# Kernel tuning notes

Measured on AMD Instinct MI355X. Metric: run time of the kernel, lower is better.

## Reference

```python
import jax, jax.numpy as jnp
import numpy as np

EPS = 1e-10


def setup_inputs() -> dict:
    key = jax.random.key(0)
    k1, k2, k3 = jax.random.split(key, 3)
    B, V = 256, 128000
    logits = jax.random.normal(k1, (B, V), dtype=jnp.float32)
    # temperatures in (0,1]; set a few entries to exactly 0 to exercise the greedy branch
    temps = jax.random.uniform(k2, (B,), dtype=jnp.float32)
    temps = temps.at[::16].set(0.0)
    # exponential(1) noise, matching torch.empty_like(probs).exponential_(1)
    exp_noise = jax.random.exponential(k3, (B, V), dtype=jnp.float32)
    return {"logits": logits, "temperatures": temps, "exp_noise": exp_noise}


def reference(logits, temperatures, exp_noise):
    logits = logits.astype(jnp.float32)
    greedy_tokens = jnp.argmax(logits, axis=-1)  # [B]
    # avoid 0-division; rows with temp==0 are overridden by the greedy branch anyway
    safe_t = jnp.where(temperatures == 0.0, 1.0, temperatures)[:, None]  # [B,1]
    probs = jax.nn.softmax(logits / safe_t, axis=-1)  # [B,V]
    # Gumbel-max style sampling: argmax of probs / Exp(1) noise
    sample_tokens = jnp.argmax(probs / (exp_noise + EPS), axis=-1)  # [B]
    return jnp.where(temperatures == 0.0, greedy_tokens, sample_tokens)
```

## Files before the change

kernel.cpp:

```cpp
#include <hip/hip_runtime.h>
#include <math.h>


__device__ __forceinline__ void amax_combine(float& v, int& i, float ov, int oi) {
    if (ov > v || (ov == v && oi < i)) { v = ov; i = oi; }
}

__global__ __launch_bounds__(1024) void draft_sampler_kernel(
    const float* __restrict__ logits,
    const float* __restrict__ temps,
    const float* __restrict__ noise,
    int* __restrict__ out,
    int V)
{
    const int row = blockIdx.x;
    const int tid = threadIdx.x;
    const int nthr = blockDim.x;
    const int lane = tid & 63;
    const int wid  = tid >> 6;
    const int nwaves = nthr >> 6;

    const size_t base = (size_t)row * (size_t)V;
    const float4* l4 = (const float4*)(logits + base);
    const int n4 = V >> 2;

    __shared__ float sv[16];
    __shared__ int   si[16];

    float bv = -INFINITY; int bi = 0x7fffffff;
    for (int j = tid; j < n4; j += nthr) {
        float4 x = l4[j];
        int k = j << 2;
        if (x.x > bv) { bv = x.x; bi = k; }
        if (x.y > bv) { bv = x.y; bi = k + 1; }
        if (x.z > bv) { bv = x.z; bi = k + 2; }
        if (x.w > bv) { bv = x.w; bi = k + 3; }
    }
    #pragma unroll
    for (int off = 32; off > 0; off >>= 1) {
        float ov = __shfl_down(bv, off, 64);
        int   oi = __shfl_down(bi, off, 64);
        amax_combine(bv, bi, ov, oi);
    }
    if (lane == 0) { sv[wid] = bv; si[wid] = bi; }
    __syncthreads();
    if (tid == 0) {
        float gv = sv[0]; int gi = si[0];
        for (int w = 1; w < nwaves; ++w) amax_combine(gv, gi, sv[w], si[w]);
        sv[0] = gv; si[0] = gi;
    }
    __syncthreads();
    const float gmax = sv[0];
    const int   gidx = si[0];

    const float t = temps[row];
    if (t == 0.0f) {
        if (tid == 0) out[row] = gidx;
        return;
    }
    const float xm = gmax / t;
    const float4* z4 = (const float4*)(noise + base);

    float rv = -INFINITY; int ri = 0x7fffffff;
    for (int j = tid; j < n4; j += nthr) {
        float4 x = l4[j];
        float4 z = z4[j];
        int k = j << 2;
        float r0 = expf(x.x / t - xm) / (z.x + 1e-10f);
        float r1 = expf(x.y / t - xm) / (z.y + 1e-10f);
        float r2 = expf(x.z / t - xm) / (z.z + 1e-10f);
        float r3 = expf(x.w / t - xm) / (z.w + 1e-10f);
        if (r0 > rv) { rv = r0; ri = k; }
        if (r1 > rv) { rv = r1; ri = k + 1; }
        if (r2 > rv) { rv = r2; ri = k + 2; }
        if (r3 > rv) { rv = r3; ri = k + 3; }
    }
    #pragma unroll
    for (int off = 32; off > 0; off >>= 1) {
        float ov = __shfl_down(rv, off, 64);
        int   oi = __shfl_down(ri, off, 64);
        amax_combine(rv, ri, ov, oi);
    }
    __syncthreads();
    if (lane == 0) { sv[wid] = rv; si[wid] = ri; }
    __syncthreads();
    if (tid == 0) {
        float gv = sv[0]; int gi = si[0];
        for (int w = 1; w < nwaves; ++w) amax_combine(gv, gi, sv[w], si[w]);
        out[row] = gi;
    }
}

extern "C" void kernel_launch(void* const* d_in, const int* in_sizes, int n_in,
                              void* d_out, int out_size, void* d_ws, size_t ws_size,
                              hipStream_t stream) {
    const float* logits = (const float*)d_in[0];
    const float* temps  = (const float*)d_in[1];
    const float* noise  = (const float*)d_in[2];
    int* out = (int*)d_out;

    const int B = in_sizes[1];
    const int V = in_sizes[0] / B;

    draft_sampler_kernel<<<B, 1024, 0, stream>>>(logits, temps, noise, out, V);
}
```

Measured before the change: 279.2 us.

## Rewrite Gumbel sampling in log space with fused single pass and split-row reduction

Replaces exp-softmax-divide with an equivalent log-domain score x*(1/t)*log2e - log2(z), so the row max is no longer needed. Greedy and sampled argmax are computed in the same single pass over logits and noise, which drops the second read of the logits. Each row is split across 8 blocks of 256 threads, with per-segment partial results written to a workspace and combined by a small second kernel. It uses fast __log2f, which may change argmax results on near-ties.

```diff
diff --git a/kernel.cpp b/kernel.cpp
--- a/kernel.cpp
+++ b/kernel.cpp
@@ -1,94 +1,106 @@
 #include <hip/hip_runtime.h>
 #include <math.h>
 
+
+#define SEGS 8
 
 __device__ __forceinline__ void amax_combine(float& v, int& i, float ov, int oi) {
     if (ov > v || (ov == v && oi < i)) { v = ov; i = oi; }
 }
 
-__global__ __launch_bounds__(1024) void draft_sampler_kernel(
+__global__ __launch_bounds__(256) void draft_pass1(
     const float* __restrict__ logits,
     const float* __restrict__ temps,
     const float* __restrict__ noise,
-    int* __restrict__ out,
+    float4* __restrict__ ws,
     int V)
 {
-    const int row = blockIdx.x;
+    const int seg = blockIdx.x;
+    const int row = blockIdx.y;
     const int tid = threadIdx.x;
-    const int nthr = blockDim.x;
     const int lane = tid & 63;
     const int wid  = tid >> 6;
-    const int nwaves = nthr >> 6;
+
+    const int n4  = V >> 2;
+    const int per = n4 / SEGS;
+    const int j0  = seg * per;
+    const int j1  = (seg == SEGS - 1) ? n4 : (j0 + per);
+
+    const float t = temps[row];
+    const float safe_t = (t == 0.0f) ? 1.0f : t;
+    const float c = (1.0f / safe_t) * 1.4426950408889634f;
 
     const size_t base = (size_t)row * (size_t)V;
     const float4* l4 = (const float4*)(logits + base);
-    const int n4 = V >> 2;
-
-    __shared__ float sv[16];
-    __shared__ int   si[16];
-
-    float bv = -INFINITY; int bi = 0x7fffffff;
-    for (int j = tid; j < n4; j += nthr) {
-        float4 x = l4[j];
-        int k = j << 2;
-        if (x.x > bv) { bv = x.x; bi = k; }
-        if (x.y > bv) { bv = x.y; bi = k + 1; }
-        if (x.z > bv) { bv = x.z; bi = k + 2; }
-        if (x.w > bv) { bv = x.w; bi = k + 3; }
-    }
-    #pragma unroll
-    for (int off = 32; off > 0; off >>= 1) {
-        float ov = __shfl_down(bv, off, 64);
-        int   oi = __shfl_down(bi, off, 64);
-        amax_combine(bv, bi, ov, oi);
-    }
-    if (lane == 0) { sv[wid] = bv; si[wid] = bi; }
-    __syncthreads();
-    if (tid == 0) {
-        float gv = sv[0]; int gi = si[0];
-        for (int w = 1; w < nwaves; ++w) amax_combine(gv, gi, sv[w], si[w]);
-        sv[0] = gv; si[0] = gi;
-    }
-    __syncthreads();
-    const float gmax = sv[0];
-    const int   gidx = si[0];
-
-    const float t = temps[row];
-    if (t == 0.0f) {
-        if (tid == 0) out[row] = gidx;
-        return;
-    }
-    const float xm = gmax / t;
     const float4* z4 = (const float4*)(noise + base);
 
-    float rv = -INFINITY; int ri = 0x7fffffff;
-    for (int j = tid; j < n4; j += nthr) {
+    float gv = -INFINITY; int gi = 0x7fffffff;
+    float sv = -INFINITY; int si = 0x7fffffff;
+
+    for (int j = j0 + tid; j < j1; j += 256) {
         float4 x = l4[j];
         float4 z = z4[j];
         int k = j << 2;
-        float r0 = expf(x.x / t - xm) / (z.x + 1e-10f);
-        float r1 = expf(x.y / t - xm) / (z.y + 1e-10f);
-        float r2 = expf(x.z / t - xm) / (z.z + 1e-10f);
-        float r3 = expf(x.w / t - xm) / (z.w + 1e-10f);
-        if (r0 > rv) { rv = r0; ri = k; }
-        if (r1 > rv) { rv = r1; ri = k + 1; }
-        if (r2 > rv) { rv = r2; ri = k + 2; }
-        if (r3 > rv) { rv = r3; ri = k + 3; }
+        if (x.x > gv) { gv = x.x; gi = k;     }
+        if (x.y > gv) { gv = x.y; gi = k + 1; }
+        if (x.z > gv) { gv = x.z; gi = k + 2; }
+        if (x.w > gv) { gv = x.w; gi = k + 3; }
+        float s0 = fmaf(x.x, c, -__log2f(z.x + 1e-10f));
+        float s1 = fmaf(x.y, c, -__log2f(z.y + 1e-10f));
+        float s2 = fmaf(x.z, c, -__log2f(z.z + 1e-10f));
+        float s3 = fmaf(x.w, c, -__log2f(z.w + 1e-10f));
+        if (s0 > sv) { sv = s0; si = k;     }
+        if (s1 > sv) { sv = s1; si = k + 1; }
+        if (s2 > sv) { sv = s2; si = k + 2; }
+        if (s3 > sv) { sv = s3; si = k + 3; }
     }
+
     #pragma unroll
     for (int off = 32; off > 0; off >>= 1) {
-        float ov = __shfl_down(rv, off, 64);
-        int   oi = __shfl_down(ri, off, 64);
-        amax_combine(rv, ri, ov, oi);
+        float ogv = __shfl_down(gv, off, 64);
+        int   ogi = __shfl_down(gi, off, 64);
+        amax_combine(gv, gi, ogv, ogi);
+        float osv = __shfl_down(sv, off, 64);
+        int   osi = __shfl_down(si, off, 64);
+        amax_combine(sv, si, osv, osi);
     }
-    __syncthreads();
-    if (lane == 0) { sv[wid] = rv; si[wid] = ri; }
+
+    __shared__ float sgv[4]; __shared__ int sgi[4];
+    __shared__ float ssv[4]; __shared__ int ssi[4];
+    if (lane == 0) { sgv[wid] = gv; sgi[wid] = gi; ssv[wid] = sv; ssi[wid] = si; }
     __syncthreads();
     if (tid == 0) {
-        float gv = sv[0]; int gi = si[0];
-        for (int w = 1; w < nwaves; ++w) amax_combine(gv, gi, sv[w], si[w]);
-        out[row] = gi;
+        float bgv = sgv[0]; int bgi = sgi[0];
+        float bsv = ssv[0]; int bsi = ssi[0];
+        #pragma unroll
+        for (int w = 1; w < 4; ++w) {
+            amax_combine(bgv, bgi, sgv[w], sgi[w]);
+            amax_combine(bsv, bsi, ssv[w], ssi[w]);
+        }
+        float4 p;
+        p.x = bgv; p.y = __int_as_float(bgi);
+        p.z = bsv; p.w = __int_as_float(bsi);
+        ws[(size_t)row * SEGS + seg] = p;
     }
+}
+
+__global__ __launch_bounds__(256) void draft_pass2(
+    const float* __restrict__ temps,
+    const float4* __restrict__ ws,
+    int* __restrict__ out,
+    int B)
+{
+    int r = blockIdx.x * blockDim.x + threadIdx.x;
+    if (r >= B) return;
+    float gv = -INFINITY; int gi = 0x7fffffff;
+    float sv = -INFINITY; int si = 0x7fffffff;
+    #pragma unroll
+    for (int s = 0; s < SEGS; ++s) {
+        float4 p = ws[(size_t)r * SEGS + s];
+        amax_combine(gv, gi, p.x, __float_as_int(p.y));
+        amax_combine(sv, si, p.z, __float_as_int(p.w));
+    }
+    out[r] = (temps[r] == 0.0f) ? gi : si;
 }
 
 extern "C" void kernel_launch(void* const* d_in, const int* in_sizes, int n_in,
@@ -102,5 +114,9 @@
     const int B = in_sizes[1];
     const int V = in_sizes[0] / B;
 
-    draft_sampler_kernel<<<B, 1024, 0, stream>>>(logits, temps, noise, out, V);
+    float4* ws = (float4*)d_ws;
+
+    dim3 grid1(SEGS, B);
+    draft_pass1<<<grid1, 256, 0, stream>>>(logits, temps, noise, ws, V);
+    draft_pass2<<<(B + 255) / 256, 256, 0, stream>>>(temps, ws, out, B);
 }
```

New measurement: 285.0 us. 1.02x slower.
